# Kernel tuning notes

Hardware: AMD Instinct MI355X
Metric: run time of the kernel (lower is better)

The kernel has to match this reference:

```python
import jax, jax.numpy as jnp
import numpy as np

N_GROUPS = 32
N_HEADS = 8
GN_EPS = 1e-5


def setup_inputs() -> dict:
    key = jax.random.key(0)
    k1, k2, k3 = jax.random.split(key, 3)
    B, C, H, W = 8, 512, 32, 32
    x = jax.random.normal(k1, (B, C, H, W), dtype=jnp.float32)
    gn_w = jnp.ones((C,), dtype=jnp.float32)
    gn_b = jnp.zeros((C,), dtype=jnp.float32)
    qkv_w = jax.random.normal(k2, (3 * C, C), dtype=jnp.float32) * 0.02
    qkv_b = jnp.zeros((3 * C,), dtype=jnp.float32)
    proj_w = jax.random.normal(k3, (C, C), dtype=jnp.float32) * 0.02
    proj_b = jnp.zeros((C,), dtype=jnp.float32)
    return {"x": x, "gn_w": gn_w, "gn_b": gn_b, "qkv_w": qkv_w,
            "qkv_b": qkv_b, "proj_w": proj_w, "proj_b": proj_b}


def reference(x, gn_w, gn_b, qkv_w, qkv_b, proj_w, proj_b):
    b, c, h, w = x.shape
    t = h * w
    xf = x.reshape(b, c, t)

    # GroupNorm(32, C) over (channel-group, spatial) dims
    xg = xf.reshape(b, N_GROUPS, (c // N_GROUPS) * t)
    mean = jnp.mean(xg, axis=-1, keepdims=True)
    var = jnp.var(xg, axis=-1, keepdims=True)
    normed = ((xg - mean) * jax.lax.rsqrt(var + GN_EPS)).reshape(b, c, t)
    normed = normed * gn_w[None, :, None] + gn_b[None, :, None]

    # 1x1 Conv1d -> matmul over channel dim
    qkv = jnp.einsum('oc,bct->bot', qkv_w, normed) + qkv_b[None, :, None]
    q, k, v = jnp.split(qkv, 3, axis=1)  # each [b, c, t]

    ch = c // N_HEADS
    scale = 1.0 / np.sqrt(np.sqrt(ch)).astype(np.float32)
    q = (q * scale).reshape(b * N_HEADS, ch, t)
    k = (k * scale).reshape(b * N_HEADS, ch, t)
    v = v.reshape(b * N_HEADS, ch, t)

    weight = jnp.einsum('bct,bcs->bts', q, k)
    weight = jax.nn.softmax(weight.astype(jnp.float32), axis=-1).astype(q.dtype)
    a = jnp.einsum('bts,bcs->bct', weight, v).reshape(b, c, t)

    # residual + 1x1 Conv2d projection
    out = jnp.einsum('oc,bct->bot', proj_w, xf + a) + proj_b[None, :, None]
    return out.reshape(b, -1, h, w)
```

## Files before the change

### kernel.cpp

```cpp
#include <hip/hip_runtime.h>

constexpr int B = 8;
constexpr int C = 512;
constexpr int T = 1024;
constexpr int CPG = 16;
constexpr int NH = 8;
constexpr int CH = 64;
constexpr float GN_EPS = 1e-5f;
constexpr float QSCALE = 0.18033688011112042f;

typedef __attribute__((ext_vector_type(4))) float f32x4;
typedef __attribute__((ext_vector_type(8))) short bf16x8;
typedef __attribute__((ext_vector_type(4))) short bf16x4;

__device__ inline short f2bf(float f) {
  union { float f; unsigned u; } v; v.f = f;
  unsigned r = (v.u + 0x7FFFu + ((v.u >> 16) & 1u)) >> 16;
  return (short)r;
}

__device__ inline unsigned cvt_pk_bf16(float a, float b) {
  unsigned r;
  asm("v_cvt_pk_bf16_f32 %0, %1, %2" : "=v"(r) : "v"(a), "v"(b));
  return r;
}

#define GLOAD16(gsrc, ldst) __builtin_amdgcn_global_load_lds( \
    (const __attribute__((address_space(1))) unsigned int*)(gsrc), \
    (__attribute__((address_space(3))) unsigned int*)(ldst), 16, 0, 0)

__global__ __launch_bounds__(256)
void gnw_kernel(const float* __restrict__ x, const float* __restrict__ gw,
                const float* __restrict__ gb, short* __restrict__ out,
                const float* __restrict__ qw, const float* __restrict__ pw,
                short* __restrict__ qwb, short* __restrict__ pwb) {
  const int bid = blockIdx.x;
  if (bid >= 256) {
    const int idx = (bid - 256) * 256 + threadIdx.x;
    constexpr int QW4 = 3 * C * C / 4;
    float4 v;
    short* dst;
    if (idx < QW4) {
      v = ((const float4*)qw)[idx];
      dst = qwb + (size_t)idx * 4;
    } else {
      v = ((const float4*)pw)[idx - QW4];
      dst = pwb + (size_t)(idx - QW4) * 4;
    }
    bf16x4 o;
    o[0] = f2bf(v.x); o[1] = f2bf(v.y); o[2] = f2bf(v.z); o[3] = f2bf(v.w);
    *(bf16x4*)dst = o;
    return;
  }
  const int b = bid >> 5;
  const int g = bid & 31;
  const float* xp = x + (size_t)(b * C + g * CPG) * T;
  const float4* x4 = (const float4*)xp;
  float s = 0.f, ss = 0.f;
  for (int i = threadIdx.x; i < CPG * T / 4; i += 256) {
    float4 v = x4[i];
    s  += v.x + v.y + v.z + v.w;
    ss += v.x * v.x + v.y * v.y + v.z * v.z + v.w * v.w;
  }
  #pragma unroll
  for (int o = 32; o; o >>= 1) {
    s  += __shfl_down(s, o);
    ss += __shfl_down(ss, o);
  }
  __shared__ float rs[4], rss[4];
  __shared__ float sm, sr;
  const int wid = threadIdx.x >> 6;
  if ((threadIdx.x & 63) == 0) { rs[wid] = s; rss[wid] = ss; }
  __syncthreads();
  if (threadIdx.x == 0) {
    float ts  = rs[0] + rs[1] + rs[2] + rs[3];
    float tss = rss[0] + rss[1] + rss[2] + rss[3];
    constexpr float inv_n = 1.f / (CPG * T);
    float mean = ts * inv_n;
    float var = tss * inv_n - mean * mean;
    sm = mean;
    sr = rsqrtf(var + GN_EPS);
  }
  __syncthreads();
  const float mean = sm, rstd = sr;

  const int tid = threadIdx.x;
  const int cl = tid >> 4;
  const int t4 = (tid & 15) * 4;
  const float cw = gw[g * CPG + cl] * rstd;
  const float cb = gb[g * CPG + cl] - mean * cw;
  __shared__ short tile[64][20];
  const int tr = tid >> 2;
  const int cq = (tid & 3) * 4;
  for (int t0 = 0; t0 < T; t0 += 64) {
    float4 v = x4[(cl * T + t0 + t4) >> 2];
    tile[t4 + 0][cl] = f2bf(v.x * cw + cb);
    tile[t4 + 1][cl] = f2bf(v.y * cw + cb);
    tile[t4 + 2][cl] = f2bf(v.z * cw + cb);
    tile[t4 + 3][cl] = f2bf(v.w * cw + cb);
    __syncthreads();
    *(bf16x4*)&out[((size_t)(b * T + t0 + tr)) * C + g * CPG + cq] =
        *(const bf16x4*)&tile[tr][cq];
    __syncthreads();
  }
}

__global__ __launch_bounds__(256)
void qkv_gemm(const short* __restrict__ Wb, const float* __restrict__ bias,
              const short* __restrict__ Xn, short* __restrict__ qb,
              short* __restrict__ kb, short* __restrict__ vb) {
  const int bid = blockIdx.x;
  const int b = bid & 7;
  const int rem = bid >> 3;
  const int o0 = (rem % 12) * 128;
  const int t0 = (rem / 12) * 64;
  const bool swap = (o0 >= 2 * C);
  __shared__ short Asm[128 * 64];
  __shared__ short Bsm[64 * 64];
  const int tid = threadIdx.x;
  const int wv = tid >> 6, lane = tid & 63;
  const int l15 = lane & 15, l4 = lane >> 4;
  const int wr = (wv >> 1) * 64;
  const int wc = (wv & 1) * 32;

  const short* gA[4]; const short* gB[2];
  char* lA[4]; char* lB[2];
  #pragma unroll
  for (int p = 0; p < 4; ++p) {
    const int off = p * 256 + tid;
    const int row = off >> 3;
    const int col = (off & 7) ^ (row & 7);
    gA[p] = Wb + (size_t)(o0 + row) * C + col * 8;
    lA[p] = (char*)Asm + (size_t)(p * 256 + (tid & ~63)) * 16;
  }
  #pragma unroll
  for (int p = 0; p < 2; ++p) {
    const int off = p * 256 + tid;
    const int row = off >> 3;
    const int col = (off & 7) ^ (row & 7);
    gB[p] = Xn + ((size_t)b * T + t0 + row) * C + col * 8;
    lB[p] = (char*)Bsm + (size_t)(p * 256 + (tid & ~63)) * 16;
  }

  f32x4 acc[8];
  #pragma unroll
  for (int i = 0; i < 8; ++i) acc[i] = f32x4{0.f, 0.f, 0.f, 0.f};

  for (int k0 = 0; k0 < C; k0 += 64) {
    #pragma unroll
    for (int p = 0; p < 4; ++p) GLOAD16(gA[p] + k0, lA[p]);
    #pragma unroll
    for (int p = 0; p < 2; ++p) GLOAD16(gB[p] + k0, lB[p]);
    __syncthreads();
    #pragma unroll
    for (int kk = 0; kk < 2; ++kk) {
      const int sw = ((kk << 2) | l4) ^ (l15 & 7);
      bf16x8 af[4], bfr[2];
      #pragma unroll
      for (int i = 0; i < 4; ++i)
        af[i] = *(const bf16x8*)&Asm[(wr + i * 16 + l15) * 64 + sw * 8];
      #pragma unroll
      for (int j = 0; j < 2; ++j)
        bfr[j] = *(const bf16x8*)&Bsm[(wc + j * 16 + l15) * 64 + sw * 8];
      __builtin_amdgcn_s_setprio(1);
      if (!swap) {
        #pragma unroll
        for (int fi = 0; fi < 4; ++fi)
          #pragma unroll
          for (int nj = 0; nj < 2; ++nj)
            acc[fi * 2 + nj] = __builtin_amdgcn_mfma_f32_16x16x32_bf16(
                af[fi], bfr[nj], acc[fi * 2 + nj], 0, 0, 0);
      } else {
        #pragma unroll
        for (int nj = 0; nj < 2; ++nj)
          #pragma unroll
          for (int fi = 0; fi < 4; ++fi)
            acc[nj * 4 + fi] = __builtin_amdgcn_mfma_f32_16x16x32_bf16(
                bfr[nj], af[fi], acc[nj * 4 + fi], 0, 0, 0);
      }
      __builtin_amdgcn_s_setprio(0);
    }
    __syncthreads();
  }

  if (!swap) {
    short* dst = (o0 < C) ? qb : kb;
    const float sc = (o0 < C) ? QSCALE : 1.0f;
    #pragma unroll
    for (int fi = 0; fi < 4; ++fi) {
      const int ob = o0 + wr + fi * 16 + l4 * 4;
      const int bh = b * NH + ((ob >> 6) & 7);
      const int cb_ = ob & 63;
      #pragma unroll
      for (int nj = 0; nj < 2; ++nj) {
        const int tg = t0 + wc + nj * 16 + l15;
        bf16x4 pk;
        #pragma unroll
        for (int r = 0; r < 4; ++r)
          pk[r] = f2bf((acc[fi * 2 + nj][r] + bias[ob + r]) * sc);
        *(bf16x4*)&dst[((size_t)bh * T + tg) * CH + cb_] = pk;
      }
    }
  } else {
    #pragma unroll
    for (int fi = 0; fi < 4; ++fi) {
      const int ob = o0 + wr + fi * 16 + l15;
      const int bh = b * NH + ((ob >> 6) & 7);
      const int cb_ = ob & 63;
      const float bo = bias[ob];
      #pragma unroll
      for (int nj = 0; nj < 2; ++nj) {
        const int tg = t0 + wc + nj * 16 + l4 * 4;
        bf16x4 pk;
        #pragma unroll
        for (int r = 0; r < 4; ++r)
          pk[r] = f2bf(acc[nj * 4 + fi][r] + bo);
        *(bf16x4*)&vb[((size_t)bh * CH + cb_) * T + tg] = pk;
      }
    }
  }
}

__global__ __launch_bounds__(256)
void attn_kernel(const short* __restrict__ qb, const short* __restrict__ kb,
                 const short* __restrict__ vb, const float* __restrict__ x,
                 short* __restrict__ res) {
  const int bh = blockIdx.x & 63;
  const int tile = blockIdx.x >> 6;
  const int b = bh >> 3, h = bh & 7;
  const int t0 = tile * 128;
  const int tid = threadIdx.x;
  const int wv = tid >> 6;
  const int lane = tid & 63;
  const int l15 = lane & 15;
  const int l4 = lane >> 4;

  const short* qh = qb + (size_t)bh * T * CH;
  const short* kh = kb + (size_t)bh * T * CH;
  const short* vh = vb + (size_t)bh * CH * T;

  extern __shared__ short smem[];
  short* ktb = smem;
  short* vtb = smem + 4 * 4096;
  short* plw = smem + 8 * 4096 + wv * 2048;

  const int sl_row[2] = { (0 * 256 + tid) >> 3, (1 * 256 + tid) >> 3 };
  const int sl_blk[2] = { (tid & 7) ^ (sl_row[0] & 7), (tid & 7) ^ (sl_row[1] & 7) };
  const int sl_lds[2] = { (0 * 256 + (tid & ~63)) * 16, (1 * 256 + (tid & ~63)) * 16 };

  bf16x8 qf[2][2];
  #pragma unroll
  for (int nj = 0; nj < 2; ++nj)
    #pragma unroll
    for (int ks = 0; ks < 2; ++ks)
      qf[nj][ks] = *(const bf16x8*)
          &qh[(size_t)(t0 + wv * 32 + nj * 16 + l15) * CH + ks * 32 + l4 * 8];

  f32x4 acc_o[2][4];
  #pragma unroll
  for (int nj = 0; nj < 2; ++nj)
    #pragma unroll
    for (int ct = 0; ct < 4; ++ct) acc_o[nj][ct] = f32x4{0.f, 0.f, 0.f, 0.f};
  float lsum[2] = {0.f, 0.f};

  #pragma unroll
  for (int j = 0; j < 2; ++j) {
    #pragma unroll
    for (int p = 0; p < 2; ++p) {
      GLOAD16(kh + (size_t)(j * 64 + sl_row[p]) * CH + sl_blk[p] * 8,
              (char*)(ktb + j * 4096) + sl_lds[p]);
      GLOAD16(vh + (size_t)sl_row[p] * T + j * 64 + sl_blk[p] * 8,
              (char*)(vtb + j * 4096) + sl_lds[p]);
    }
  }

  for (int g = 0; g < 8; ++g) {
    const int pr = (g & 1) * 2;
    __syncthreads();
    if (g < 7) {
      const int tt = 2 * g + 2;
      #pragma unroll
      for (int j = 0; j < 2; ++j) {
        const int bf = (pr ^ 2) + j;
        #pragma unroll
        for (int p = 0; p < 2; ++p) {
          GLOAD16(kh + (size_t)((tt + j) * 64 + sl_row[p]) * CH + sl_blk[p] * 8,
                  (char*)(ktb + bf * 4096) + sl_lds[p]);
          GLOAD16(vh + (size_t)sl_row[p] * T + (tt + j) * 64 + sl_blk[p] * 8,
                  (char*)(vtb + bf * 4096) + sl_lds[p]);
        }
      }
    }

    #pragma unroll
    for (int j = 0; j < 2; ++j) {
      const short* ktc = ktb + (pr + j) * 4096;
      const short* vtc = vtb + (pr + j) * 4096;

      f32x4 accs[2][4];
      #pragma unroll
      for (int nj = 0; nj < 2; ++nj)
        #pragma unroll
        for (int nt = 0; nt < 4; ++nt) accs[nj][nt] = f32x4{0.f, 0.f, 0.f, 0.f};
      __builtin_amdgcn_s_setprio(1);
      #pragma unroll
      for (int ks = 0; ks < 2; ++ks) {
        #pragma unroll
        for (int nt = 0; nt < 4; ++nt) {
          bf16x8 kf = *(const bf16x8*)
              &ktc[(nt * 16 + l15) * 64 + (((ks << 2) | l4) ^ (l15 & 7)) * 8];
          accs[0][nt] = __builtin_amdgcn_mfma_f32_16x16x32_bf16(kf, qf[0][ks], accs[0][nt], 0, 0, 0);
          accs[1][nt] = __builtin_amdgcn_mfma_f32_16x16x32_bf16(kf, qf[1][ks], accs[1][nt], 0, 0, 0);
        }
      }
      __builtin_amdgcn_s_setprio(0);

      f32x4 p4[2][4];
      #pragma unroll
      for (int nj = 0; nj < 2; ++nj) {
        #pragma unroll
        for (int nt = 0; nt < 4; ++nt)
          #pragma unroll
          for (int r = 0; r < 4; ++r)
            p4[nj][nt][r] = __builtin_amdgcn_exp2f(accs[nj][nt][r]);
        f32x4 sv;
        #pragma unroll
        for (int r = 0; r < 4; ++r)
          sv[r] = (p4[nj][0][r] + p4[nj][1][r]) + (p4[nj][2][r] + p4[nj][3][r]);
        lsum[nj] += (sv[0] + sv[1]) + (sv[2] + sv[3]);
        #pragma unroll
        for (int nt = 0; nt < 4; ++nt) {
          uint2 w;
          w.x = cvt_pk_bf16(p4[nj][nt][0], p4[nj][nt][1]);
          w.y = cvt_pk_bf16(p4[nj][nt][2], p4[nj][nt][3]);
          *(uint2*)&plw[nj * 1024 + l15 * 64 +
                        ((nt * 2 + (l4 >> 1)) ^ (l15 & 7)) * 8 + (l4 & 1) * 4] = w;
        }
      }

      __builtin_amdgcn_s_setprio(1);
      #pragma unroll
      for (int ks = 0; ks < 2; ++ks) {
        const int psl = (((ks << 2) | l4) ^ (l15 & 7)) * 8;
        bf16x8 pf0 = *(const bf16x8*)&plw[l15 * 64 + psl];
        bf16x8 pf1 = *(const bf16x8*)&plw[1024 + l15 * 64 + psl];
        #pragma unroll
        for (int ct = 0; ct < 4; ++ct) {
          bf16x8 vf = *(const bf16x8*)
              &vtc[(ct * 16 + l15) * 64 + (((ks << 2) | l4) ^ (l15 & 7)) * 8];
          acc_o[0][ct] = __builtin_amdgcn_mfma_f32_16x16x32_bf16(vf, pf0, acc_o[0][ct], 0, 0, 0);
          acc_o[1][ct] = __builtin_amdgcn_mfma_f32_16x16x32_bf16(vf, pf1, acc_o[1][ct], 0, 0, 0);
        }
      }
      __builtin_amdgcn_s_setprio(0);
    }
  }

  #pragma unroll
  for (int nj = 0; nj < 2; ++nj) {
    float l = lsum[nj];
    l += __shfl_xor(l, 16);
    l += __shfl_xor(l, 32);
    const float inv = 1.f / l;
    const int trow = t0 + wv * 32 + nj * 16 + l15;
    #pragma unroll
    for (int ct = 0; ct < 4; ++ct) {
      const int cbase = h * CH + ct * 16 + l4 * 4;
      bf16x4 pk;
      #pragma unroll
      for (int r = 0; r < 4; ++r) {
        const float xv = x[((size_t)(b * C + cbase + r)) * T + trow];
        pk[r] = f2bf(acc_o[nj][ct][r] * inv + xv);
      }
      *(bf16x4*)&res[((size_t)(b * T + trow)) * C + cbase] = pk;
    }
  }
}

__global__ __launch_bounds__(256)
void proj_gemm(const short* __restrict__ Wp, const float* __restrict__ bias,
               const short* __restrict__ Rs, float* __restrict__ out) {
  const int bid = blockIdx.x;
  const int b = bid & 7;
  const int rem = bid >> 3;
  const int o0 = (rem & 3) * 128;
  const int t0 = (rem >> 2) * 64;
  __shared__ short Asm[128 * 64];
  __shared__ short Bsm[64 * 64];
  const int tid = threadIdx.x;
  const int wv = tid >> 6, lane = tid & 63;
  const int l15 = lane & 15, l4 = lane >> 4;
  const int wr = (wv >> 1) * 64;
  const int wc = (wv & 1) * 32;

  const short* gA[4]; const short* gB[2];
  char* lA[4]; char* lB[2];
  #pragma unroll
  for (int p = 0; p < 4; ++p) {
    const int off = p * 256 + tid;
    const int row = off >> 3;
    const int col = (off & 7) ^ (row & 7);
    gA[p] = Wp + (size_t)(o0 + row) * C + col * 8;
    lA[p] = (char*)Asm + (size_t)(p * 256 + (tid & ~63)) * 16;
  }
  #pragma unroll
  for (int p = 0; p < 2; ++p) {
    const int off = p * 256 + tid;
    const int row = off >> 3;
    const int col = (off & 7) ^ (row & 7);
    gB[p] = Rs + ((size_t)b * T + t0 + row) * C + col * 8;
    lB[p] = (char*)Bsm + (size_t)(p * 256 + (tid & ~63)) * 16;
  }

  f32x4 acc[2][4];
  #pragma unroll
  for (int i = 0; i < 2; ++i)
    #pragma unroll
    for (int j = 0; j < 4; ++j) acc[i][j] = f32x4{0.f, 0.f, 0.f, 0.f};

  for (int k0 = 0; k0 < C; k0 += 64) {
    #pragma unroll
    for (int p = 0; p < 4; ++p) GLOAD16(gA[p] + k0, lA[p]);
    #pragma unroll
    for (int p = 0; p < 2; ++p) GLOAD16(gB[p] + k0, lB[p]);
    __syncthreads();
    #pragma unroll
    for (int kk = 0; kk < 2; ++kk) {
      const int sw = ((kk << 2) | l4) ^ (l15 & 7);
      bf16x8 af[4], bfr[2];
      #pragma unroll
      for (int i = 0; i < 4; ++i)
        af[i] = *(const bf16x8*)&Asm[(wr + i * 16 + l15) * 64 + sw * 8];
      #pragma unroll
      for (int j = 0; j < 2; ++j)
        bfr[j] = *(const bf16x8*)&Bsm[(wc + j * 16 + l15) * 64 + sw * 8];
      __builtin_amdgcn_s_setprio(1);
      #pragma unroll
      for (int nj = 0; nj < 2; ++nj)
        #pragma unroll
        for (int fi = 0; fi < 4; ++fi)
          acc[nj][fi] = __builtin_amdgcn_mfma_f32_16x16x32_bf16(
              bfr[nj], af[fi], acc[nj][fi], 0, 0, 0);
      __builtin_amdgcn_s_setprio(0);
    }
    __syncthreads();
  }

  #pragma unroll
  for (int fi = 0; fi < 4; ++fi) {
    const int o = o0 + wr + fi * 16 + l15;
    const float bo = bias[o];
    #pragma unroll
    for (int nj = 0; nj < 2; ++nj) {
      const int tg = t0 + wc + nj * 16 + l4 * 4;
      f32x4 vo;
      #pragma unroll
      for (int r = 0; r < 4; ++r) vo[r] = acc[nj][fi][r] + bo;
      *(f32x4*)&out[((size_t)(b * C + o)) * T + tg] = vo;
    }
  }
}

extern "C" void kernel_launch(void* const* d_in, const int* in_sizes, int n_in,
                              void* d_out, int out_size, void* d_ws, size_t ws_size,
                              hipStream_t stream) {
  const float* x      = (const float*)d_in[0];
  const float* gn_w   = (const float*)d_in[1];
  const float* gn_b   = (const float*)d_in[2];
  const float* qkv_w  = (const float*)d_in[3];
  const float* qkv_b  = (const float*)d_in[4];
  const float* proj_w = (const float*)d_in[5];
  const float* proj_b = (const float*)d_in[6];
  float* out = (float*)d_out;

  constexpr size_t MB = 1 << 20;
  char* w = (char*)d_ws;
  short* normed = (short*)w;
  short* qbuf   = (short*)(w + 8 * MB);
  short* kbuf   = (short*)(w + 16 * MB);
  short* vbuf   = (short*)(w + 24 * MB);
  short* resb   = (short*)(w + 32 * MB);
  short* qwb    = (short*)(w + 40 * MB);
  short* pwb    = (short*)(w + 40 * MB + (size_t)3 * C * C * 2);

  gnw_kernel<<<dim3(1280), 256, 0, stream>>>(x, gn_w, gn_b, normed,
                                             qkv_w, proj_w, qwb, pwb);
  qkv_gemm<<<dim3(1536), 256, 0, stream>>>(qwb, qkv_b, normed, qbuf, kbuf, vbuf);
  attn_kernel<<<dim3(B * NH * (T / 128)), 256, 81920, stream>>>(qbuf, kbuf, vbuf, x, resb);
  proj_gemm<<<dim3(512), 256, 0, stream>>>(pwb, proj_b, resb, out);
}
```

Measured before the change: 93.87 us.

## Shrink attention LDS to double-buffered single key tiles for higher occupancy

The attention kernel goes from dynamic shared memory holding four 64-key K/V tiles (two tiles per stage, double-buffered) to static arrays holding two single 64-key tiles in a plain double buffer. The loop now runs 16 iterations with one block barrier each instead of 8. Total LDS per block drops from 80 KB to 48 KB, which should let more blocks reside per CU. The cost is twice as many barriers and less prefetch lookahead per sync.

```diff
diff --git a/kernel.cpp b/kernel.cpp
--- a/kernel.cpp
+++ b/kernel.cpp
@@ -239,14 +239,14 @@
   const short* kh = kb + (size_t)bh * T * CH;
   const short* vh = vb + (size_t)bh * CH * T;
 
-  extern __shared__ short smem[];
-  short* ktb = smem;
-  short* vtb = smem + 4 * 4096;
-  short* plw = smem + 8 * 4096 + wv * 2048;
+  __shared__ short kt[2][64][64];
+  __shared__ short vt[2][64][64];
+  __shared__ short pl[4][2][16][64];
+  short* plw = &pl[wv][0][0][0];
 
   const int sl_row[2] = { (0 * 256 + tid) >> 3, (1 * 256 + tid) >> 3 };
   const int sl_blk[2] = { (tid & 7) ^ (sl_row[0] & 7), (tid & 7) ^ (sl_row[1] & 7) };
-  const int sl_lds[2] = { (0 * 256 + (tid & ~63)) * 16, (1 * 256 + (tid & ~63)) * 16 };
+  const int sl_lds[2] = { (0 * 256 + (tid & ~63)) * 8, (1 * 256 + (tid & ~63)) * 8 };
 
   bf16x8 qf[2][2];
   #pragma unroll
@@ -264,96 +264,83 @@
   float lsum[2] = {0.f, 0.f};
 
   #pragma unroll
-  for (int j = 0; j < 2; ++j) {
-    #pragma unroll
-    for (int p = 0; p < 2; ++p) {
-      GLOAD16(kh + (size_t)(j * 64 + sl_row[p]) * CH + sl_blk[p] * 8,
-              (char*)(ktb + j * 4096) + sl_lds[p]);
-      GLOAD16(vh + (size_t)sl_row[p] * T + j * 64 + sl_blk[p] * 8,
-              (char*)(vtb + j * 4096) + sl_lds[p]);
-    }
-  }
-
-  for (int g = 0; g < 8; ++g) {
-    const int pr = (g & 1) * 2;
-    __syncthreads();
-    if (g < 7) {
-      const int tt = 2 * g + 2;
-      #pragma unroll
-      for (int j = 0; j < 2; ++j) {
-        const int bf = (pr ^ 2) + j;
-        #pragma unroll
-        for (int p = 0; p < 2; ++p) {
-          GLOAD16(kh + (size_t)((tt + j) * 64 + sl_row[p]) * CH + sl_blk[p] * 8,
-                  (char*)(ktb + bf * 4096) + sl_lds[p]);
-          GLOAD16(vh + (size_t)sl_row[p] * T + (tt + j) * 64 + sl_blk[p] * 8,
-                  (char*)(vtb + bf * 4096) + sl_lds[p]);
-        }
-      }
-    }
-
-    #pragma unroll
-    for (int j = 0; j < 2; ++j) {
-      const short* ktc = ktb + (pr + j) * 4096;
-      const short* vtc = vtb + (pr + j) * 4096;
-
-      f32x4 accs[2][4];
-      #pragma unroll
-      for (int nj = 0; nj < 2; ++nj)
-        #pragma unroll
-        for (int nt = 0; nt < 4; ++nt) accs[nj][nt] = f32x4{0.f, 0.f, 0.f, 0.f};
-      __builtin_amdgcn_s_setprio(1);
-      #pragma unroll
-      for (int ks = 0; ks < 2; ++ks) {
-        #pragma unroll
-        for (int nt = 0; nt < 4; ++nt) {
-          bf16x8 kf = *(const bf16x8*)
-              &ktc[(nt * 16 + l15) * 64 + (((ks << 2) | l4) ^ (l15 & 7)) * 8];
-          accs[0][nt] = __builtin_amdgcn_mfma_f32_16x16x32_bf16(kf, qf[0][ks], accs[0][nt], 0, 0, 0);
-          accs[1][nt] = __builtin_amdgcn_mfma_f32_16x16x32_bf16(kf, qf[1][ks], accs[1][nt], 0, 0, 0);
-        }
-      }
-      __builtin_amdgcn_s_setprio(0);
-
-      f32x4 p4[2][4];
-      #pragma unroll
-      for (int nj = 0; nj < 2; ++nj) {
-        #pragma unroll
-        for (int nt = 0; nt < 4; ++nt)
-          #pragma unroll
-          for (int r = 0; r < 4; ++r)
-            p4[nj][nt][r] = __builtin_amdgcn_exp2f(accs[nj][nt][r]);
-        f32x4 sv;
+  for (int p = 0; p < 2; ++p) {
+    GLOAD16(kh + (size_t)sl_row[p] * CH + sl_blk[p] * 8, (char*)&kt[0][0][0] + sl_lds[p] * 2);
+    GLOAD16(vh + (size_t)sl_row[p] * T + sl_blk[p] * 8, (char*)&vt[0][0][0] + sl_lds[p] * 2);
+  }
+
+  for (int it = 0; it < 16; ++it) {
+    const int cur = it & 1;
+    __syncthreads();
+    if (it < 15) {
+      const int s1 = (it + 1) * 64;
+      #pragma unroll
+      for (int p = 0; p < 2; ++p) {
+        GLOAD16(kh + (size_t)(s1 + sl_row[p]) * CH + sl_blk[p] * 8,
+                (char*)&kt[cur ^ 1][0][0] + sl_lds[p] * 2);
+        GLOAD16(vh + (size_t)sl_row[p] * T + s1 + sl_blk[p] * 8,
+                (char*)&vt[cur ^ 1][0][0] + sl_lds[p] * 2);
+      }
+    }
+    const short* ktc = &kt[cur][0][0];
+    const short* vtc = &vt[cur][0][0];
+
+    f32x4 accs[2][4];
+    #pragma unroll
+    for (int nj = 0; nj < 2; ++nj)
+      #pragma unroll
+      for (int nt = 0; nt < 4; ++nt) accs[nj][nt] = f32x4{0.f, 0.f, 0.f, 0.f};
+    __builtin_amdgcn_s_setprio(1);
+    #pragma unroll
+    for (int ks = 0; ks < 2; ++ks) {
+      #pragma unroll
+      for (int nt = 0; nt < 4; ++nt) {
+        bf16x8 kf = *(const bf16x8*)
+            &ktc[(nt * 16 + l15) * 64 + (((ks << 2) | l4) ^ (l15 & 7)) * 8];
+        accs[0][nt] = __builtin_amdgcn_mfma_f32_16x16x32_bf16(kf, qf[0][ks], accs[0][nt], 0, 0, 0);
+        accs[1][nt] = __builtin_amdgcn_mfma_f32_16x16x32_bf16(kf, qf[1][ks], accs[1][nt], 0, 0, 0);
+      }
+    }
+    __builtin_amdgcn_s_setprio(0);
+
+    f32x4 p4[2][4];
+    #pragma unroll
+    for (int nj = 0; nj < 2; ++nj) {
+      #pragma unroll
+      for (int nt = 0; nt < 4; ++nt)
         #pragma unroll
         for (int r = 0; r < 4; ++r)
-          sv[r] = (p4[nj][0][r] + p4[nj][1][r]) + (p4[nj][2][r] + p4[nj][3][r]);
-        lsum[nj] += (sv[0] + sv[1]) + (sv[2] + sv[3]);
-        #pragma unroll
-        for (int nt = 0; nt < 4; ++nt) {
-          uint2 w;
-          w.x = cvt_pk_bf16(p4[nj][nt][0], p4[nj][nt][1]);
-          w.y = cvt_pk_bf16(p4[nj][nt][2], p4[nj][nt][3]);
-          *(uint2*)&plw[nj * 1024 + l15 * 64 +
-                        ((nt * 2 + (l4 >> 1)) ^ (l15 & 7)) * 8 + (l4 & 1) * 4] = w;
-        }
-      }
-
-      __builtin_amdgcn_s_setprio(1);
-      #pragma unroll
-      for (int ks = 0; ks < 2; ++ks) {
-        const int psl = (((ks << 2) | l4) ^ (l15 & 7)) * 8;
-        bf16x8 pf0 = *(const bf16x8*)&plw[l15 * 64 + psl];
-        bf16x8 pf1 = *(const bf16x8*)&plw[1024 + l15 * 64 + psl];
-        #pragma unroll
-        for (int ct = 0; ct < 4; ++ct) {
-          bf16x8 vf = *(const bf16x8*)
-              &vtc[(ct * 16 + l15) * 64 + (((ks << 2) | l4) ^ (l15 & 7)) * 8];
-          acc_o[0][ct] = __builtin_amdgcn_mfma_f32_16x16x32_bf16(vf, pf0, acc_o[0][ct], 0, 0, 0);
-          acc_o[1][ct] = __builtin_amdgcn_mfma_f32_16x16x32_bf16(vf, pf1, acc_o[1][ct], 0, 0, 0);
-        }
-      }
-      __builtin_amdgcn_s_setprio(0);
-    }
+          p4[nj][nt][r] = __builtin_amdgcn_exp2f(accs[nj][nt][r]);
+      f32x4 sv;
+      #pragma unroll
+      for (int r = 0; r < 4; ++r)
+        sv[r] = (p4[nj][0][r] + p4[nj][1][r]) + (p4[nj][2][r] + p4[nj][3][r]);
+      lsum[nj] += (sv[0] + sv[1]) + (sv[2] + sv[3]);
+      #pragma unroll
+      for (int nt = 0; nt < 4; ++nt) {
+        uint2 w;
+        w.x = cvt_pk_bf16(p4[nj][nt][0], p4[nj][nt][1]);
+        w.y = cvt_pk_bf16(p4[nj][nt][2], p4[nj][nt][3]);
+        *(uint2*)&plw[nj * 1024 + l15 * 64 +
+                      ((nt * 2 + (l4 >> 1)) ^ (l15 & 7)) * 8 + (l4 & 1) * 4] = w;
+      }
+    }
+
+    __builtin_amdgcn_s_setprio(1);
+    #pragma unroll
+    for (int ks = 0; ks < 2; ++ks) {
+      const int psl = (((ks << 2) | l4) ^ (l15 & 7)) * 8;
+      bf16x8 pf0 = *(const bf16x8*)&plw[l15 * 64 + psl];
+      bf16x8 pf1 = *(const bf16x8*)&plw[1024 + l15 * 64 + psl];
+      #pragma unroll
+      for (int ct = 0; ct < 4; ++ct) {
+        bf16x8 vf = *(const bf16x8*)
+            &vtc[(ct * 16 + l15) * 64 + (((ks << 2) | l4) ^ (l15 & 7)) * 8];
+        acc_o[0][ct] = __builtin_amdgcn_mfma_f32_16x16x32_bf16(vf, pf0, acc_o[0][ct], 0, 0, 0);
+        acc_o[1][ct] = __builtin_amdgcn_mfma_f32_16x16x32_bf16(vf, pf1, acc_o[1][ct], 0, 0, 0);
+      }
+    }
+    __builtin_amdgcn_s_setprio(0);
   }
 
   #pragma unroll
@@ -486,6 +473,6 @@
   gnw_kernel<<<dim3(1280), 256, 0, stream>>>(x, gn_w, gn_b, normed,
                                              qkv_w, proj_w, qwb, pwb);
   qkv_gemm<<<dim3(1536), 256, 0, stream>>>(qwb, qkv_b, normed, qbuf, kbuf, vbuf);
-  attn_kernel<<<dim3(B * NH * (T / 128)), 256, 81920, stream>>>(qbuf, kbuf, vbuf, x, resb);
+  attn_kernel<<<dim3(B * NH * (T / 128)), 256, 0, stream>>>(qbuf, kbuf, vbuf, x, resb);
   proj_gemm<<<dim3(512), 256, 0, stream>>>(pwb, proj_b, resb, out);
 }
```

After: 86.25 us. 1.09x faster.
